# Kernel optimization log

Hardware: AMD Instinct MI355X
Metric: run time of the kernel (lower is better)

The kernel has to match this reference:

```python
import jax, jax.numpy as jnp
import numpy as np

S, B, F, D, DF, NH, FH = 1152, 2, 128, 1024, 2048, 8, 4
SEP = 1024
EPS = 1e-5

def ln(x, g, b):
    m = x.mean(-1, keepdims=True)
    v = ((x - m) ** 2).mean(-1, keepdims=True)
    return (x - m) * jax.lax.rsqrt(v + EPS) * g + b

def mha(q, k, v, wi, bi, wo, bo, nh):
    # torch MultiheadAttention, batch_first=False: inputs (L, N, E)
    E = q.shape[-1]
    hd = E // nh
    qh = (q @ wi[:E].T + bi[:E]).reshape(q.shape[0], -1, nh, hd)
    kh = (k @ wi[E:2 * E].T + bi[E:2 * E]).reshape(k.shape[0], -1, nh, hd)
    vh = (v @ wi[2 * E:].T + bi[2 * E:]).reshape(k.shape[0], -1, nh, hd)
    s = jnp.einsum('qnhd,knhd->nhqk', qh, kh) / jnp.sqrt(jnp.float32(hd))
    a = jax.nn.softmax(s, axis=-1)
    o = jnp.einsum('nhqk,knhd->qnhd', a, vh).reshape(q.shape[0], -1, E)
    return o @ wo.T + bo

def setup_inputs() -> dict:
    key = jax.random.key(0)
    it = iter(jax.random.split(key, 40))
    def p(shape, s=0.02):
        return jax.random.normal(next(it), shape, jnp.float32) * s
    z = lambda *sh: jnp.zeros(sh, jnp.float32)
    o = lambda *sh: jnp.ones(sh, jnp.float32)
    return dict(
        src=jax.random.normal(next(it), (S, B, F), jnp.float32),
        sep=SEP,
        sa_wi=p((3 * D, D)), sa_bi=z(3 * D), sa_wo=p((D, D)), sa_bo=z(D),
        fa_wi=p((3 * F, F)), fa_bi=z(3 * F), fa_wo=p((F, F)), fa_bo=z(F),
        pl1_w=p((F, 1)), pl1_b=z(F),
        pl2_w=p((DF, F)), pl2_b=z(DF),
        pl3_w=p((1, DF)), pl3_b=z(1),
        pl4_w=p((DF, F)), pl4_b=z(DF),
        pl5_w=p((D, DF)), pl5_b=z(D),
        pl6_w=p((DF, D)), pl6_b=z(DF),
        pl7_w=p((D, DF)), pl7_b=z(D),
        l1_w=p((DF, D)), l1_b=z(DF),
        l2_w=p((F, DF)), l2_b=z(F),
        pn1_g=o(F), pn1_b=z(F),
        pn2_g=o(D), pn2_b=z(D),
        n1_g=o(D), n1_b=z(D),
        n2_g=o(F), n2_b=z(F),
    )

def _forward(src, sa_wi, sa_bi, sa_wo, sa_bo, fa_wi, fa_bi, fa_wo, fa_bo,
             pl1_w, pl1_b, pl2_w, pl2_b, pl3_w, pl3_b, pl4_w, pl4_b,
             pl5_w, pl5_b, pl6_w, pl6_b, pl7_w, pl7_b, l1_w, l1_b, l2_w, l2_b,
             pn1_g, pn1_b, pn2_g, pn2_b, n1_g, n1_b, n2_g, n2_b, sep):
    Sn, Bn, Fn = src.shape
    relu = jax.nn.relu
    # feature-wise attention: 'b h w -> w (b h) 1'
    x = jnp.transpose(src, (2, 0, 1)).reshape(Fn, Sn * Bn, 1)
    x = x @ pl1_w.T + pl1_b                       # (F, S*B, emsize_f)
    x = mha(x, x, x, fa_wi, fa_bi, fa_wo, fa_bo, FH)
    x = relu(x @ pl2_w.T + pl2_b) @ pl3_w.T + pl3_b  # (F, S*B, 1)
    x = jnp.transpose(x.reshape(Fn, Sn, Bn), (1, 2, 0))  # 'w (b h) 1 -> b h w'
    src1 = ln(x + src, pn1_g, pn1_b)              # (S, B, F)
    src1_ = relu(src1 @ pl4_w.T + pl4_b) @ pl5_w.T + pl5_b  # (S, B, D)
    li = src1_[:sep]
    sl = mha(li, li, li, sa_wi, sa_bi, sa_wo, sa_bo, NH)
    sl = ln(sl + li, pn2_g, pn2_b)
    sl_ = relu(sl @ pl6_w.T + pl6_b) @ pl7_w.T + pl7_b
    sl_ = ln(sl_, pn2_g, pn2_b) + sl
    sr = mha(src1_[sep:], sl_, sl_, sa_wi, sa_bi, sa_wo, sa_bo, NH)
    src2 = jnp.concatenate([sl, sr], axis=0)      # (S, B, D)
    so = ln(src2 + src1_, n1_g, n1_b)
    ff = relu(so @ l1_w.T + l1_b) @ l2_w.T + l2_b  # (S, B, F)
    return ln(src1 + ff, n2_g, n2_b)

def reference(src, sa_wi, sa_bi, sa_wo, sa_bo, fa_wi, fa_bi, fa_wo, fa_bo,
              pl1_w, pl1_b, pl2_w, pl2_b, pl3_w, pl3_b, pl4_w, pl4_b,
              pl5_w, pl5_b, pl6_w, pl6_b, pl7_w, pl7_b, l1_w, l1_b, l2_w, l2_b,
              pn1_g, pn1_b, pn2_g, pn2_b, n1_g, n1_b, n2_g, n2_b, sep):
    return _forward(src, sa_wi, sa_bi, sa_wo, sa_bo, fa_wi, fa_bi, fa_wo, fa_bo,
                    pl1_w, pl1_b, pl2_w, pl2_b, pl3_w, pl3_b, pl4_w, pl4_b,
                    pl5_w, pl5_b, pl6_w, pl6_b, pl7_w, pl7_b, l1_w, l1_b,
                    l2_w, l2_b, pn1_g, pn1_b, pn2_g, pn2_b, n1_g, n1_b,
                    n2_g, n2_b, sep)
```

## Files before the change

### kernel.cpp

```cpp
#include <hip/hip_runtime.h>

using s16x8 = __attribute__((ext_vector_type(8))) short;
using f32x4 = __attribute__((ext_vector_type(4))) float;
typedef unsigned short ushort_t;

__device__ __forceinline__ unsigned short f2bf(float f) {
    union { float f; unsigned u; } v; v.f = f;
    unsigned u = v.u + 0x7FFFu + ((v.u >> 16) & 1u);
    return (unsigned short)(u >> 16);
}
__device__ __forceinline__ float bf2f(unsigned short h) {
    union { unsigned u; float f; } v; v.u = ((unsigned)h) << 16;
    return v.f;
}

__device__ __forceinline__ float block_reduce(float v, int op, float* lds) {
    const int lane = threadIdx.x & 63;
    const int w    = threadIdx.x >> 6;
    const int nw   = blockDim.x >> 6;
#pragma unroll
    for (int off = 32; off > 0; off >>= 1) {
        float o = __shfl_down(v, off, 64);
        v = op ? fmaxf(v, o) : (v + o);
    }
    __syncthreads();
    if (lane == 0) lds[w] = v;
    __syncthreads();
    float r = lds[0];
    for (int i = 1; i < nw; i++) r = op ? fmaxf(r, lds[i]) : (r + lds[i]);
    return r;
}

__device__ __forceinline__ void load_lds16(const void* g, void* l) {
    __builtin_amdgcn_global_load_lds(
        (const __attribute__((address_space(1))) unsigned int*)g,
        (__attribute__((address_space(3))) unsigned int*)l, 16, 0, 0);
}

struct CvtArgs { const float* src[8]; ushort_t* dst[8]; int end[8]; };

__global__ __launch_bounds__(256)
void cvt_all(CvtArgs a)
{
    int i = blockIdx.x * 256 + threadIdx.x;
    int j = 0;
    while (j < 8 && i >= a.end[j]) j++;
    if (j >= 8) return;
    int li = i - (j ? a.end[j - 1] : 0);
    float4 v = *(const float4*)&a.src[j][(size_t)li * 4];
    ushort_t u[4] = { f2bf(v.x), f2bf(v.y), f2bf(v.z), f2bf(v.w) };
    *(uint2*)&a.dst[j][(size_t)li * 4] = *(uint2*)u;
}

template<bool BKN, bool RELU>
__global__ __launch_bounds__(256, 2)
void gemm_bf16(const ushort_t* __restrict__ A, const ushort_t* __restrict__ B,
               const float* __restrict__ bias, ushort_t* __restrict__ C,
               int M, int N, int K, int lda, int ldb, int ldc,
               long sAz, long sBz, long sCz, long sA2, long sB2, long sC2,
               int zshift, float alpha)
{
    __shared__ ushort_t As[128 * 32];
    __shared__ ushort_t Bs[128 * 32];

    const int tid = threadIdx.x;
    const int z   = blockIdx.z;
    const int z1  = z & ((1 << zshift) - 1);
    const int z2  = z >> zshift;
    const int m0  = blockIdx.x * 128;
    const int n0  = blockIdx.y * 128;

    const ushort_t* Ab = A + (size_t)z1 * sAz + (size_t)z2 * sA2 + (size_t)m0 * lda;
    const ushort_t* Bb = B + (size_t)z1 * sBz + (size_t)z2 * sB2;

    const int wave = tid >> 6, lane = tid & 63;
    const int wm = (wave & 1) * 64, wn = (wave >> 1) * 64;
    const int mi = lane & 15, quad = lane >> 4;

    f32x4 acc[4][4];
#pragma unroll
    for (int i = 0; i < 4; i++)
#pragma unroll
        for (int j = 0; j < 4; j++) acc[i][j] = (f32x4)0.f;

    const int r_0 = tid >> 2,           g_0 = (tid & 3) ^ ((r_0 >> 1) & 3);
    const int r_1 = (tid + 256) >> 2,   g_1 = (tid & 3) ^ ((r_1 >> 1) & 3);
    const int bk = tid >> 3, bn = (tid & 7) * 16;

    for (int k0 = 0; k0 < K; k0 += 32) {
        load_lds16(Ab + (size_t)r_0 * lda + k0 + g_0 * 8, &As[tid * 8]);
        load_lds16(Ab + (size_t)r_1 * lda + k0 + g_1 * 8, &As[(tid + 256) * 8]);
        if (!BKN) {
            const ushort_t* Bb2 = Bb + (size_t)n0 * ldb;
            load_lds16(Bb2 + (size_t)r_0 * ldb + k0 + g_0 * 8, &Bs[tid * 8]);
            load_lds16(Bb2 + (size_t)r_1 * ldb + k0 + g_1 * 8, &Bs[(tid + 256) * 8]);
        } else {
#pragma unroll
            for (int c = 0; c < 2; c++) {
                s16x8 v = *(const s16x8*)(Bb + (size_t)(k0 + bk) * ldb + n0 + bn + c * 8);
#pragma unroll
                for (int j = 0; j < 8; j++) {
                    int nr = bn + c * 8 + j;
                    Bs[nr * 32 + (((bk >> 3) ^ ((nr >> 1) & 3)) * 8) + (bk & 7)] = (ushort_t)v[j];
                }
            }
        }
        __syncthreads();

        s16x8 af[4], bfr[4];
#pragma unroll
        for (int t = 0; t < 4; t++) {
            int r = wm + t * 16 + mi;
            af[t] = *(const s16x8*)&As[r * 32 + ((quad ^ ((r >> 1) & 3)) * 8)];
        }
#pragma unroll
        for (int t = 0; t < 4; t++) {
            int r = wn + t * 16 + mi;
            bfr[t] = *(const s16x8*)&Bs[r * 32 + ((quad ^ ((r >> 1) & 3)) * 8)];
        }
#pragma unroll
        for (int tm = 0; tm < 4; tm++)
#pragma unroll
            for (int tn = 0; tn < 4; tn++)
                acc[tm][tn] = __builtin_amdgcn_mfma_f32_16x16x32_bf16(af[tm], bfr[tn], acc[tm][tn], 0, 0, 0);
        __syncthreads();
    }

#pragma unroll
    for (int tn = 0; tn < 4; tn++) {
        int col = n0 + wn + tn * 16 + mi;
        float bv = bias ? bias[col] : 0.f;
#pragma unroll
        for (int tm = 0; tm < 4; tm++) {
#pragma unroll
            for (int r = 0; r < 4; r++) {
                int row = m0 + wm + tm * 16 + quad * 4 + r;
                float v = acc[tm][tn][r] * alpha + bv;
                if (RELU) v = fmaxf(v, 0.f);
                C[(size_t)z1 * sCz + (size_t)z2 * sC2 + (size_t)row * ldc + col] = f2bf(v);
            }
        }
    }
}

__global__ void precomp1(const float* __restrict__ fa_wi, const float* __restrict__ fa_bi,
                         const float* __restrict__ pl1_w, const float* __restrict__ pl1_b,
                         float* __restrict__ consts)
{
    int j = threadIdx.x;
    if (j < 384) {
        float u = 0.f, v = 0.f;
        for (int k = 0; k < 128; k++) {
            float w = fa_wi[j * 128 + k];
            u = fmaf(w, pl1_w[k], u);
            v = fmaf(w, pl1_b[k], v);
        }
        consts[j]       = u;
        consts[512 + j] = v + fa_bi[j];
    }
}

__global__ void precomp2(const float* __restrict__ fa_wo, const float* __restrict__ fa_bo,
                         float* __restrict__ consts)
{
    int tid = threadIdx.x;
    const float* u = consts;
    const float* v = consts + 512;
    if (tid < 16) {
        int h = tid >> 2, w = tid & 3;
        const float* ql = (w < 2) ? u : v;
        const float* kr = ((w & 1) == 0) ? u : v;
        float acc = 0.f;
        for (int d = 0; d < 32; d++) acc += ql[h * 32 + d] * kr[128 + h * 32 + d];
        consts[1024 + tid] = acc * 0.17677669529663687f;
    }
#pragma unroll
    for (int h = 0; h < 4; h++) {
        float acc = 0.f;
        for (int d = 0; d < 32; d++)
            acc = fmaf(fa_wo[tid * 128 + h * 32 + d], u[256 + h * 32 + d], acc);
        consts[1088 + h * 128 + tid] = acc;
    }
    float c0 = fa_bo[tid];
    for (int idx = 0; idx < 128; idx++)
        c0 = fmaf(fa_wo[tid * 128 + idx], v[256 + idx], c0);
    consts[1600 + tid] = c0;
}

__global__ void precomp3(const float* __restrict__ pl2_w, const float* __restrict__ pl2_b,
                         const float* __restrict__ consts, ushort_t* __restrict__ Gb)
{
    int m = blockIdx.x * 256 + threadIdx.x;
    const float* wv = consts + 1088;
    const float* c0 = consts + 1600;
    float a0 = 0.f, ah[4] = {0.f, 0.f, 0.f, 0.f};
    for (int j = 0; j < 128; j++) {
        float w = pl2_w[m * 128 + j];
        ah[0] = fmaf(w, wv[0 * 128 + j], ah[0]);
        ah[1] = fmaf(w, wv[1 * 128 + j], ah[1]);
        ah[2] = fmaf(w, wv[2 * 128 + j], ah[2]);
        ah[3] = fmaf(w, wv[3 * 128 + j], ah[3]);
        a0    = fmaf(w, c0[j], a0);
    }
    ushort_t* row = Gb + m * 32;
#pragma unroll
    for (int h = 0; h < 4; h++) row[h] = f2bf(ah[h]);
    row[4] = f2bf(a0 + pl2_b[m]);
#pragma unroll
    for (int j = 5; j < 32; j++) row[j] = 0;
}

__global__ __launch_bounds__(256, 3)
void feat_mlp_ln(const float* __restrict__ src, const float* __restrict__ consts,
                 const ushort_t* __restrict__ Gb, const float* __restrict__ pl3_w,
                 const float* __restrict__ pl3_b, const float* __restrict__ pn1_g,
                 const float* __restrict__ pn1_b, ushort_t* __restrict__ src1)
{
    __shared__ ushort_t As[128 * 32];
    __shared__ ushort_t Bs[256 * 32];
    __shared__ float sv[128];
    __shared__ float ypart[2][128];
    __shared__ float red[4];

    const int n   = blockIdx.x;
    const int tid = threadIdx.x;
    const int f   = tid & 127;
    const int hp  = tid >> 7;

    *(uint4*)&As[tid * 16]     = (uint4){0, 0, 0, 0};
    *(uint4*)&As[tid * 16 + 8] = (uint4){0, 0, 0, 0};
    if (tid < 128) sv[f] = src[n * 128 + f];
    __syncthreads();

    const float si = sv[f];
    const bool act = (tid < 128);
    float S1 = block_reduce(act ? si : 0.f, 0, red);
    float S2 = block_reduce(act ? si * si : 0.f, 0, red);
    float S3 = block_reduce(act ? si * si * si : 0.f, 0, red);
    float S4 = block_reduce(act ? si * si * si * si : 0.f, 0, red);
    float amax = block_reduce(act ? fabsf(si) : 0.f, 1, red);

    float ph[2];
#pragma unroll
    for (int hh = 0; hh < 2; hh++) {
        const int h = hp * 2 + hh;
        ph[hh] = consts[1024 + h * 4 + 0] * si + consts[1024 + h * 4 + 2];
    }
    float pmax = block_reduce(fmaxf(fabsf(ph[0]), fabsf(ph[1])), 1, red);

    float tt[2];
    if (pmax * amax < 0.25f) {
#pragma unroll
        for (int hh = 0; hh < 2; hh++) {
            float p = ph[hh];
            float num = fmaf(p, fmaf(p, fmaf(p, S4 * (1.f / 6.f), 0.5f * S3), S2), S1);
            float den = fmaf(p, fmaf(p, fmaf(p, S3 * (1.f / 6.f), 0.5f * S2), S1), 128.f);
            tt[hh] = num / den;
        }
    } else {
        float smax = block_reduce(act ? si : -3.4e38f, 1, red);
        float smin = -block_reduce(act ? -si : -3.4e38f, 1, red);
#pragma unroll
        for (int hh = 0; hh < 2; hh++) {
            float p = ph[hh];
            float m = fmaxf(p * smax, p * smin);
            float l = 0.f, t = 0.f;
            for (int j = 0; j < 128; j++) {
                float e = __expf(fmaf(p, sv[j], -m));
                l += e; t = fmaf(e, sv[j], t);
            }
            tt[hh] = t / l;
        }
    }

    {
        int base = f * 32 + (((f >> 1) & 3) * 8);
        As[base + hp * 2 + 0] = f2bf(tt[0]);
        As[base + hp * 2 + 1] = f2bf(tt[1]);
        if (act) As[base + 4] = 0x3F80;
    }
    __syncthreads();

    const int wave = tid >> 6, lane = tid & 63;
    const int wm = (wave & 1) * 64, wn = (wave >> 1) * 64;
    const int mi = lane & 15, quad = lane >> 4;

    s16x8 af[4];
#pragma unroll
    for (int t = 0; t < 4; t++) {
        int r = wm + t * 16 + mi;
        af[t] = *(const s16x8*)&As[r * 32 + ((quad ^ ((r >> 1) & 3)) * 8)];
    }

    float partial[4][4];
#pragma unroll
    for (int i = 0; i < 4; i++)
#pragma unroll
        for (int j = 0; j < 4; j++) partial[i][j] = 0.f;

    for (int cchunk = 0; cchunk < 8; cchunk++) {
        const ushort_t* Gc = Gb + cchunk * 256 * 32;
#pragma unroll
        for (int p = 0; p < 4; p++) {
            int ci = tid + p * 256;
            int r  = ci >> 2;
            int g  = (ci & 3) ^ ((r >> 1) & 3);
            load_lds16(Gc + (size_t)r * 32 + g * 8, &Bs[ci * 8]);
        }
        __syncthreads();

#pragma unroll
        for (int sub = 0; sub < 2; sub++) {
            s16x8 bfr[4];
#pragma unroll
            for (int t = 0; t < 4; t++) {
                int r = sub * 128 + wn + t * 16 + mi;
                bfr[t] = *(const s16x8*)&Bs[r * 32 + ((quad ^ ((r >> 1) & 3)) * 8)];
            }

            f32x4 acc[4][4];
#pragma unroll
            for (int tm = 0; tm < 4; tm++)
#pragma unroll
                for (int tn = 0; tn < 4; tn++)
                    acc[tm][tn] = __builtin_amdgcn_mfma_f32_16x16x32_bf16(af[tm], bfr[tn], (f32x4)0.f, 0, 0, 0);

#pragma unroll
            for (int tn = 0; tn < 4; tn++) {
                float w = pl3_w[cchunk * 256 + sub * 128 + wn + tn * 16 + mi];
#pragma unroll
                for (int tm = 0; tm < 4; tm++)
#pragma unroll
                    for (int r = 0; r < 4; r++)
                        partial[tm][r] = fmaf(fmaxf(acc[tm][tn][r], 0.f), w, partial[tm][r]);
            }
        }
        __syncthreads();
    }

#pragma unroll
    for (int tm = 0; tm < 4; tm++)
#pragma unroll
        for (int r = 0; r < 4; r++) {
            float v = partial[tm][r];
            v += __shfl_xor(v, 8);
            v += __shfl_xor(v, 4);
            v += __shfl_xor(v, 2);
            v += __shfl_xor(v, 1);
            if (mi == 0) ypart[wave >> 1][wm + tm * 16 + quad * 4 + r] = v;
        }
    __syncthreads();

    float yv = 0.f;
    if (act)
        yv = ypart[0][f] + ypart[1][f] + pl3_b[0] + sv[f];
    float s  = block_reduce(yv, 0, red);
    float ss = block_reduce(yv * yv, 0, red);
    float mean = s * (1.f / 128.f);
    float var  = ss * (1.f / 128.f) - mean * mean;
    float inv  = rsqrtf(var + 1e-5f);
    if (act)
        src1[n * 128 + f] = f2bf((yv - mean) * inv * pn1_g[f] + pn1_b[f]);
}

template<bool OUTF32>
__global__ void ln_bf16(const ushort_t* __restrict__ a, const ushort_t* __restrict__ b,
                        const ushort_t* __restrict__ post, const float* __restrict__ g,
                        const float* __restrict__ beta, void* __restrict__ out, int D)
{
    __shared__ float red[4];
    const size_t row = blockIdx.x;
    const int tid = threadIdx.x;
    const int nit = D / blockDim.x;
    const ushort_t* ap = a + row * D;
    const ushort_t* bp = b ? b + row * D : nullptr;
    float xr[4];
    float s = 0.f, ss = 0.f;
    for (int i = 0; i < nit; i++) {
        int idx = i * blockDim.x + tid;
        float x = bf2f(ap[idx]) + (bp ? bf2f(bp[idx]) : 0.f);
        xr[i] = x; s += x; ss = fmaf(x, x, ss);
    }
    s  = block_reduce(s, 0, red);
    ss = block_reduce(ss, 0, red);
    float mean = s / D, var = ss / D - mean * mean;
    float inv = rsqrtf(var + 1e-5f);
    const ushort_t* pp = post ? post + row * D : nullptr;
    for (int i = 0; i < nit; i++) {
        int idx = i * blockDim.x + tid;
        float v = (xr[i] - mean) * inv * g[idx] + beta[idx];
        if (pp) v += bf2f(pp[idx]);
        if (OUTF32) ((float*)out)[row * D + idx] = v;
        else        ((ushort_t*)out)[row * D + idx] = f2bf(v);
    }
}

__global__ void ln_cat(const ushort_t* __restrict__ a1, const ushort_t* __restrict__ a2,
                       int split, const ushort_t* __restrict__ b,
                       const float* __restrict__ g, const float* __restrict__ beta,
                       ushort_t* __restrict__ out, int D)
{
    __shared__ float red[4];
    const int row = blockIdx.x;
    const int tid = threadIdx.x;
    const int nit = D / blockDim.x;
    const ushort_t* ap = (row < split) ? a1 + (size_t)row * D : a2 + (size_t)(row - split) * D;
    const ushort_t* bp = b + (size_t)row * D;
    float xr[4];
    float s = 0.f, ss = 0.f;
    for (int i = 0; i < nit; i++) {
        int idx = i * blockDim.x + tid;
        float x = bf2f(ap[idx]) + bf2f(bp[idx]);
        xr[i] = x; s += x; ss = fmaf(x, x, ss);
    }
    s  = block_reduce(s, 0, red);
    ss = block_reduce(ss, 0, red);
    float mean = s / D, var = ss / D - mean * mean;
    float inv = rsqrtf(var + 1e-5f);
    for (int i = 0; i < nit; i++) {
        int idx = i * blockDim.x + tid;
        out[(size_t)row * D + idx] = f2bf((xr[i] - mean) * inv * g[idx] + beta[idx]);
    }
}

__global__ __launch_bounds__(256)
void softmax_bf16(ushort_t* __restrict__ S)
{
    __shared__ float red[4];
    const size_t row = blockIdx.x;
    ushort_t* p = S + row * 1024;
    const int tid = threadIdx.x;
    uint2 u = *(const uint2*)&p[tid * 4];
    ushort_t* us = (ushort_t*)&u;
    float xr[4];
    float mx = -3.4e38f;
#pragma unroll
    for (int i = 0; i < 4; i++) { xr[i] = bf2f(us[i]); mx = fmaxf(mx, xr[i]); }
    mx = block_reduce(mx, 1, red);
    float sum = 0.f;
#pragma unroll
    for (int i = 0; i < 4; i++) { xr[i] = __expf(xr[i] - mx); sum += xr[i]; }
    sum = block_reduce(sum, 0, red);
    float inv = 1.f / sum;
#pragma unroll
    for (int i = 0; i < 4; i++) us[i] = f2bf(xr[i] * inv);
    *(uint2*)&p[tid * 4] = u;
}

static inline void gemm_go(hipStream_t s, const ushort_t* A, const ushort_t* B,
                           const float* bias, ushort_t* C,
                           int M, int N, int K, int lda, int ldb, int ldc,
                           long sAz, long sBz, long sCz, int Z, float alpha,
                           bool bkn, bool relu,
                           long sA2 = 0, long sB2 = 0, long sC2 = 0, int zshift = 0)
{
    dim3 g(M / 128, N / 128, Z), b(256);
    if (bkn)       gemm_bf16<true,  false><<<g, b, 0, s>>>(A, B, bias, C, M, N, K, lda, ldb, ldc, sAz, sBz, sCz, sA2, sB2, sC2, zshift, alpha);
    else if (relu) gemm_bf16<false, true ><<<g, b, 0, s>>>(A, B, bias, C, M, N, K, lda, ldb, ldc, sAz, sBz, sCz, sA2, sB2, sC2, zshift, alpha);
    else           gemm_bf16<false, false><<<g, b, 0, s>>>(A, B, bias, C, M, N, K, lda, ldb, ldc, sAz, sBz, sCz, sA2, sB2, sC2, zshift, alpha);
}

extern "C" void kernel_launch(void* const* d_in, const int* in_sizes, int n_in,
                              void* d_out, int out_size, void* d_ws, size_t ws_size,
                              hipStream_t stream)
{
    const float* src   = (const float*)d_in[0];
    const float* sa_wi = (const float*)d_in[2];
    const float* sa_bi = (const float*)d_in[3];
    const float* sa_wo = (const float*)d_in[4];
    const float* sa_bo = (const float*)d_in[5];
    const float* fa_wi = (const float*)d_in[6];
    const float* fa_bi = (const float*)d_in[7];
    const float* fa_wo = (const float*)d_in[8];
    const float* fa_bo = (const float*)d_in[9];
    const float* pl1_w = (const float*)d_in[10];
    const float* pl1_b = (const float*)d_in[11];
    const float* pl2_w = (const float*)d_in[12];
    const float* pl2_b = (const float*)d_in[13];
    const float* pl3_w = (const float*)d_in[14];
    const float* pl3_b = (const float*)d_in[15];
    const float* pl4_w = (const float*)d_in[16];
    const float* pl4_b = (const float*)d_in[17];
    const float* pl5_w = (const float*)d_in[18];
    const float* pl5_b = (const float*)d_in[19];
    const float* pl6_w = (const float*)d_in[20];
    const float* pl6_b = (const float*)d_in[21];
    const float* pl7_w = (const float*)d_in[22];
    const float* pl7_b = (const float*)d_in[23];
    const float* l1_w  = (const float*)d_in[24];
    const float* l1_b  = (const float*)d_in[25];
    const float* l2_w  = (const float*)d_in[26];
    const float* l2_b  = (const float*)d_in[27];
    const float* pn1_g = (const float*)d_in[28];
    const float* pn1_b = (const float*)d_in[29];
    const float* pn2_g = (const float*)d_in[30];
    const float* pn2_b = (const float*)d_in[31];
    const float* n1_g  = (const float*)d_in[32];
    const float* n1_b  = (const float*)d_in[33];
    const float* n2_g  = (const float*)d_in[34];
    const float* n2_b  = (const float*)d_in[35];

    float* ws  = (float*)d_ws;
    float* out = (float*)d_out;

    float* CONSTS = ws;
    ushort_t* wsb = (ushort_t*)(ws + 16384);
    ushort_t* SAWIb  = wsb + 0;
    ushort_t* SAWOb  = wsb + 3145728;
    ushort_t* PL4b   = wsb + 4194304;
    ushort_t* PL5b   = wsb + 4456448;
    ushort_t* PL6b   = wsb + 6553600;
    ushort_t* PL7b   = wsb + 8650752;
    ushort_t* L1b    = wsb + 10747904;
    ushort_t* L2b    = wsb + 12845056;
    ushort_t* Gbb    = wsb + 13107200;
    ushort_t* SRC1b  = wsb + 13172736;
    ushort_t* HBIGb  = wsb + 13467648;
    ushort_t* SRC1_b = wsb + 18186240;
    ushort_t* QKVb   = wsb + 20545536;
    ushort_t* SBUFb  = wsb + 27623424;
    ushort_t* OBUFb  = wsb + 44400640;
    ushort_t* SLb    = wsb + 46497792;
    ushort_t* SLPb   = wsb + 48594944;
    ushort_t* SOb    = wsb + 50692096;
    ushort_t* FFb    = wsb + 53051392;

    {
        CvtArgs a;
        const float* srcs[8] = { sa_wi, sa_wo, pl4_w, pl5_w, pl6_w, pl7_w, l1_w, l2_w };
        ushort_t*    dsts[8] = { SAWIb, SAWOb, PL4b, PL5b, PL6b, PL7b, L1b, L2b };
        int          ns[8]   = { 3145728, 1048576, 262144, 2097152, 2097152, 2097152, 2097152, 262144 };
        int cum = 0;
        for (int i = 0; i < 8; i++) { a.src[i] = srcs[i]; a.dst[i] = dsts[i]; cum += ns[i] / 4; a.end[i] = cum; }
        cvt_all<<<(cum + 255) / 256, 256, 0, stream>>>(a);
    }

    precomp1<<<1, 384, 0, stream>>>(fa_wi, fa_bi, pl1_w, pl1_b, CONSTS);
    precomp2<<<1, 128, 0, stream>>>(fa_wo, fa_bo, CONSTS);
    precomp3<<<8, 256, 0, stream>>>(pl2_w, pl2_b, CONSTS, Gbb);
    feat_mlp_ln<<<2304, 256, 0, stream>>>(src, CONSTS, Gbb, pl3_w, pl3_b, pn1_g, pn1_b, SRC1b);

    gemm_go(stream, SRC1b, PL4b, pl4_b, HBIGb, 2304, 2048, 128, 128, 128, 2048, 0, 0, 0, 1, 1.f, false, true);
    gemm_go(stream, HBIGb, PL5b, pl5_b, SRC1_b, 2304, 1024, 2048, 2048, 2048, 1024, 0, 0, 0, 1, 1.f, false, false);

    gemm_go(stream, SRC1_b, SAWIb, sa_bi, QKVb, 2304, 3072, 1024, 1024, 1024, 3072, 0, 0, 0, 1, 1.f, false, false);
    const float iscale = 0.08838834764831845f;
    gemm_go(stream, QKVb, QKVb + 1024, nullptr, SBUFb,
            1024, 1024, 128, 6144, 6144, 1024, 128, 128, 1048576, 16, iscale, false, false,
            3072, 3072, 8388608, 3);
    softmax_bf16<<<16384, 256, 0, stream>>>(SBUFb);
    gemm_go(stream, SBUFb, QKVb + 2048, nullptr, OBUFb,
            1024, 128, 1024, 1024, 6144, 2048, 1048576, 128, 128, 16, 1.f, true, false,
            8388608, 3072, 1024, 3);
    gemm_go(stream, OBUFb, SAWOb, sa_bo, HBIGb, 2048, 1024, 1024, 1024, 1024, 1024, 0, 0, 0, 1, 1.f, false, false);
    ln_bf16<false><<<2048, 256, 0, stream>>>(HBIGb, SRC1_b, nullptr, pn2_g, pn2_b, SLb, 1024);

    gemm_go(stream, SLb, PL6b, pl6_b, HBIGb, 2048, 2048, 1024, 1024, 1024, 2048, 0, 0, 0, 1, 1.f, false, true);
    gemm_go(stream, HBIGb, PL7b, pl7_b, OBUFb, 2048, 1024, 2048, 2048, 2048, 1024, 0, 0, 0, 1, 1.f, false, false);
    ln_bf16<false><<<2048, 256, 0, stream>>>(OBUFb, nullptr, SLb, pn2_g, pn2_b, SLPb, 1024);

    ushort_t* KV2 = SBUFb;
    ushort_t* S2  = SBUFb + 4456448;
    ushort_t* SR  = SBUFb + 6553600;
    gemm_go(stream, SLPb, SAWIb + 1024 * 1024, sa_bi + 1024, KV2, 2048, 2048, 1024, 1024, 1024, 2048, 0, 0, 0, 1, 1.f, false, false);
    gemm_go(stream, QKVb + 2048 * 3072, KV2, nullptr, S2,
            128, 1024, 128, 6144, 4096, 1024, 128, 128, 131072, 16, iscale, false, false,
            3072, 2048, 1048576, 3);
    softmax_bf16<<<2048, 256, 0, stream>>>(S2);
    gemm_go(stream, S2, KV2 + 1024, nullptr, OBUFb,
            128, 128, 1024, 1024, 4096, 2048, 131072, 128, 128, 16, 1.f, true, false,
            1048576, 2048, 1024, 3);
    gemm_go(stream, OBUFb, SAWOb, sa_bo, SR, 256, 1024, 1024, 1024, 1024, 1024, 0, 0, 0, 1, 1.f, false, false);

    ln_cat<<<2304, 256, 0, stream>>>(SLb, SR, 2048, SRC1_b, n1_g, n1_b, SOb, 1024);

    gemm_go(stream, SOb, L1b, l1_b, HBIGb, 2304, 2048, 1024, 1024, 1024, 2048, 0, 0, 0, 1, 1.f, false, true);
    gemm_go(stream, HBIGb, L2b, l2_b, FFb, 2304, 128, 2048, 2048, 2048, 128, 0, 0, 0, 1, 1.f, false, false);
    ln_bf16<true><<<2304, 128, 0, stream>>>(FFb, SRC1b, nullptr, n2_g, n2_b, out, 128);
}
```

Measured before the change: 665.4 us.

## Pre-transpose V for attention GEMMs and shrink feature MLP K padding

Adds a transpose kernel that writes V in N-major layout, so the attention P·V GEMMs can use the async LDS-load path instead of the scalar scattered B-transposed load. The BKN template variant is removed. Separately, the feature-MLP kernel now packs its tiny K=5 operand into 8-wide rows, preloads the whole G matrix and pl3 weights into LDS once, and runs a single-tile MFMA loop instead of 32-wide padded chunks with repeated syncs. Costs two extra transpose launches and more LDS per block in feat_mlp_ln, which may lower occupancy.

Result: faster. 639.3 us (-3.9%).

```diff
diff --git a/kernel.cpp b/kernel.cpp
--- a/kernel.cpp
+++ b/kernel.cpp
@@ -52,7 +52,7 @@
     *(uint2*)&a.dst[j][(size_t)li * 4] = *(uint2*)u;
 }
 
-template<bool BKN, bool RELU>
+template<bool RELU>
 __global__ __launch_bounds__(256, 2)
 void gemm_bf16(const ushort_t* __restrict__ A, const ushort_t* __restrict__ B,
                const float* __restrict__ bias, ushort_t* __restrict__ C,
@@ -71,7 +71,7 @@
     const int n0  = blockIdx.y * 128;
 
     const ushort_t* Ab = A + (size_t)z1 * sAz + (size_t)z2 * sA2 + (size_t)m0 * lda;
-    const ushort_t* Bb = B + (size_t)z1 * sBz + (size_t)z2 * sB2;
+    const ushort_t* Bb = B + (size_t)z1 * sBz + (size_t)z2 * sB2 + (size_t)n0 * ldb;
 
     const int wave = tid >> 6, lane = tid & 63;
     const int wm = (wave & 1) * 64, wn = (wave >> 1) * 64;
@@ -85,26 +85,12 @@
 
     const int r_0 = tid >> 2,           g_0 = (tid & 3) ^ ((r_0 >> 1) & 3);
     const int r_1 = (tid + 256) >> 2,   g_1 = (tid & 3) ^ ((r_1 >> 1) & 3);
-    const int bk = tid >> 3, bn = (tid & 7) * 16;
 
     for (int k0 = 0; k0 < K; k0 += 32) {
         load_lds16(Ab + (size_t)r_0 * lda + k0 + g_0 * 8, &As[tid * 8]);
         load_lds16(Ab + (size_t)r_1 * lda + k0 + g_1 * 8, &As[(tid + 256) * 8]);
-        if (!BKN) {
-            const ushort_t* Bb2 = Bb + (size_t)n0 * ldb;
-            load_lds16(Bb2 + (size_t)r_0 * ldb + k0 + g_0 * 8, &Bs[tid * 8]);
-            load_lds16(Bb2 + (size_t)r_1 * ldb + k0 + g_1 * 8, &Bs[(tid + 256) * 8]);
-        } else {
-#pragma unroll
-            for (int c = 0; c < 2; c++) {
-                s16x8 v = *(const s16x8*)(Bb + (size_t)(k0 + bk) * ldb + n0 + bn + c * 8);
-#pragma unroll
-                for (int j = 0; j < 8; j++) {
-                    int nr = bn + c * 8 + j;
-                    Bs[nr * 32 + (((bk >> 3) ^ ((nr >> 1) & 3)) * 8) + (bk & 7)] = (ushort_t)v[j];
-                }
-            }
-        }
+        load_lds16(Bb + (size_t)r_0 * ldb + k0 + g_0 * 8, &Bs[tid * 8]);
+        load_lds16(Bb + (size_t)r_1 * ldb + k0 + g_1 * 8, &Bs[(tid + 256) * 8]);
         __syncthreads();
 
         s16x8 af[4], bfr[4];
@@ -140,6 +126,32 @@
                 C[(size_t)z1 * sCz + (size_t)z2 * sC2 + (size_t)row * ldc + col] = f2bf(v);
             }
         }
+    }
+}
+
+__global__ __launch_bounds__(256)
+void transp128(const ushort_t* __restrict__ in, ushort_t* __restrict__ out,
+               int ldin, long inz1, long inz2, long outz)
+{
+    __shared__ ushort_t T[64][136];
+    const int z = blockIdx.z, z1 = z & 7, z2 = z >> 3;
+    const int n0 = blockIdx.x * 64;
+    const ushort_t* ip = in + (size_t)z1 * inz1 + (size_t)z2 * inz2;
+    const int rr = threadIdx.x >> 2, cg = (threadIdx.x & 3) * 32;
+#pragma unroll
+    for (int c = 0; c < 4; c++) {
+        s16x8 v = *(const s16x8*)(ip + (size_t)(n0 + rr) * ldin + cg + c * 8);
+        *(s16x8*)&T[rr][cg + c * 8] = v;
+    }
+    __syncthreads();
+    const int d = threadIdx.x >> 1, j0 = (threadIdx.x & 1) * 32;
+    ushort_t* op = out + (size_t)z * outz + (size_t)d * 1024 + n0 + j0;
+#pragma unroll
+    for (int c = 0; c < 4; c++) {
+        s16x8 v;
+#pragma unroll
+        for (int j = 0; j < 8; j++) v[j] = (short)T[j0 + c * 8 + j][d];
+        *(s16x8*)(op + c * 8) = v;
     }
 }
 
@@ -202,12 +214,12 @@
         ah[3] = fmaf(w, wv[3 * 128 + j], ah[3]);
         a0    = fmaf(w, c0[j], a0);
     }
-    ushort_t* row = Gb + m * 32;
+    ushort_t row[8];
 #pragma unroll
     for (int h = 0; h < 4; h++) row[h] = f2bf(ah[h]);
     row[4] = f2bf(a0 + pl2_b[m]);
-#pragma unroll
-    for (int j = 5; j < 32; j++) row[j] = 0;
+    row[5] = row[6] = row[7] = 0;
+    *(uint4*)&Gb[m * 8] = *(uint4*)row;
 }
 
 __global__ __launch_bounds__(256, 3)
@@ -216,24 +228,31 @@
                  const float* __restrict__ pl3_b, const float* __restrict__ pn1_g,
                  const float* __restrict__ pn1_b, ushort_t* __restrict__ src1)
 {
-    __shared__ ushort_t As[128 * 32];
-    __shared__ ushort_t Bs[256 * 32];
-    __shared__ float sv[128];
-    __shared__ float ypart[2][128];
-    __shared__ float red[4];
+    __shared__ ushort_t Gs[2048 * 8];
+    __shared__ ushort_t Ts[128 * 8];
+    __shared__ float    wlds[2048];
+    __shared__ float    sv[128];
+    __shared__ float    ypart[2][128];
+    __shared__ float    red[4];
 
     const int n   = blockIdx.x;
     const int tid = threadIdx.x;
     const int f   = tid & 127;
     const int hp  = tid >> 7;
-
-    *(uint4*)&As[tid * 16]     = (uint4){0, 0, 0, 0};
-    *(uint4*)&As[tid * 16 + 8] = (uint4){0, 0, 0, 0};
-    if (tid < 128) sv[f] = src[n * 128 + f];
+    const bool act = (tid < 128);
+
+#pragma unroll
+    for (int p = 0; p < 8; p++) {
+        int ci = tid + p * 256;
+        load_lds16(Gb + (size_t)ci * 8, &Gs[ci * 8]);
+    }
+    load_lds16(pl3_w + tid * 4,          &wlds[tid * 4]);
+    load_lds16(pl3_w + (tid + 256) * 4,  &wlds[(tid + 256) * 4]);
+
+    if (act) sv[f] = src[n * 128 + f];
     __syncthreads();
 
     const float si = sv[f];
-    const bool act = (tid < 128);
     float S1 = block_reduce(act ? si : 0.f, 0, red);
     float S2 = block_reduce(act ? si * si : 0.f, 0, red);
     float S3 = block_reduce(act ? si * si * si : 0.f, 0, red);
@@ -273,23 +292,23 @@
         }
     }
 
-    {
-        int base = f * 32 + (((f >> 1) & 3) * 8);
-        As[base + hp * 2 + 0] = f2bf(tt[0]);
-        As[base + hp * 2 + 1] = f2bf(tt[1]);
-        if (act) As[base + 4] = 0x3F80;
+    Ts[f * 8 + hp * 2 + 0] = f2bf(tt[0]);
+    Ts[f * 8 + hp * 2 + 1] = f2bf(tt[1]);
+    if (act) {
+        Ts[f * 8 + 4] = 0x3F80;
+        Ts[f * 8 + 5] = 0; Ts[f * 8 + 6] = 0; Ts[f * 8 + 7] = 0;
     }
     __syncthreads();
 
     const int wave = tid >> 6, lane = tid & 63;
-    const int wm = (wave & 1) * 64, wn = (wave >> 1) * 64;
+    const int mhalf = wave >> 1, wm = (wave & 1) * 64;
     const int mi = lane & 15, quad = lane >> 4;
 
     s16x8 af[4];
 #pragma unroll
     for (int t = 0; t < 4; t++) {
-        int r = wm + t * 16 + mi;
-        af[t] = *(const s16x8*)&As[r * 32 + ((quad ^ ((r >> 1) & 3)) * 8)];
+        s16x8 v = *(const s16x8*)&Ts[(wm + t * 16 + mi) * 8];
+        af[t] = (quad == 0) ? v : (s16x8)0;
     }
 
     float partial[4][4];
@@ -298,44 +317,20 @@
 #pragma unroll
         for (int j = 0; j < 4; j++) partial[i][j] = 0.f;
 
-    for (int cchunk = 0; cchunk < 8; cchunk++) {
-        const ushort_t* Gc = Gb + cchunk * 256 * 32;
-#pragma unroll
-        for (int p = 0; p < 4; p++) {
-            int ci = tid + p * 256;
-            int r  = ci >> 2;
-            int g  = (ci & 3) ^ ((r >> 1) & 3);
-            load_lds16(Gc + (size_t)r * 32 + g * 8, &Bs[ci * 8]);
-        }
-        __syncthreads();
-
-#pragma unroll
-        for (int sub = 0; sub < 2; sub++) {
-            s16x8 bfr[4];
-#pragma unroll
-            for (int t = 0; t < 4; t++) {
-                int r = sub * 128 + wn + t * 16 + mi;
-                bfr[t] = *(const s16x8*)&Bs[r * 32 + ((quad ^ ((r >> 1) & 3)) * 8)];
-            }
-
-            f32x4 acc[4][4];
-#pragma unroll
-            for (int tm = 0; tm < 4; tm++)
-#pragma unroll
-                for (int tn = 0; tn < 4; tn++)
-                    acc[tm][tn] = __builtin_amdgcn_mfma_f32_16x16x32_bf16(af[tm], bfr[tn], (f32x4)0.f, 0, 0, 0);
-
-#pragma unroll
-            for (int tn = 0; tn < 4; tn++) {
-                float w = pl3_w[cchunk * 256 + sub * 128 + wn + tn * 16 + mi];
-#pragma unroll
-                for (int tm = 0; tm < 4; tm++)
-#pragma unroll
-                    for (int r = 0; r < 4; r++)
-                        partial[tm][r] = fmaf(fmaxf(acc[tm][tn][r], 0.f), w, partial[tm][r]);
-            }
-        }
-        __syncthreads();
+#pragma unroll 2
+    for (int mt = 0; mt < 64; mt++) {
+        const int m0 = mhalf * 1024 + mt * 16;
+        s16x8 bfr = *(const s16x8*)&Gs[(m0 + mi) * 8];
+        f32x4 acc[4];
+#pragma unroll
+        for (int tm = 0; tm < 4; tm++)
+            acc[tm] = __builtin_amdgcn_mfma_f32_16x16x32_bf16(af[tm], bfr, (f32x4)0.f, 0, 0, 0);
+        float w = wlds[m0 + mi];
+#pragma unroll
+        for (int tm = 0; tm < 4; tm++)
+#pragma unroll
+            for (int r = 0; r < 4; r++)
+                partial[tm][r] = fmaf(fmaxf(acc[tm][r], 0.f), w, partial[tm][r]);
     }
 
 #pragma unroll
@@ -347,7 +342,7 @@
             v += __shfl_xor(v, 4);
             v += __shfl_xor(v, 2);
             v += __shfl_xor(v, 1);
-            if (mi == 0) ypart[wave >> 1][wm + tm * 16 + quad * 4 + r] = v;
+            if (mi == 0) ypart[mhalf][wm + tm * 16 + quad * 4 + r] = v;
         }
     __syncthreads();
 
@@ -451,13 +446,12 @@
                            const float* bias, ushort_t* C,
                            int M, int N, int K, int lda, int ldb, int ldc,
                            long sAz, long sBz, long sCz, int Z, float alpha,
-                           bool bkn, bool relu,
+                           bool relu,
                            long sA2 = 0, long sB2 = 0, long sC2 = 0, int zshift = 0)
 {
     dim3 g(M / 128, N / 128, Z), b(256);
-    if (bkn)       gemm_bf16<true,  false><<<g, b, 0, s>>>(A, B, bias, C, M, N, K, lda, ldb, ldc, sAz, sBz, sCz, sA2, sB2, sC2, zshift, alpha);
-    else if (relu) gemm_bf16<false, true ><<<g, b, 0, s>>>(A, B, bias, C, M, N, K, lda, ldb, ldc, sAz, sBz, sCz, sA2, sB2, sC2, zshift, alpha);
-    else           gemm_bf16<false, false><<<g, b, 0, s>>>(A, B, bias, C, M, N, K, lda, ldb, ldc, sAz, sBz, sCz, sA2, sB2, sC2, zshift, alpha);
+    if (relu) gemm_bf16<true ><<<g, b, 0, s>>>(A, B, bias, C, M, N, K, lda, ldb, ldc, sAz, sBz, sCz, sA2, sB2, sC2, zshift, alpha);
+    else      gemm_bf16<false><<<g, b, 0, s>>>(A, B, bias, C, M, N, K, lda, ldb, ldc, sAz, sBz, sCz, sA2, sB2, sC2, zshift, alpha);
 }
 
 extern "C" void kernel_launch(void* const* d_in, const int* in_sizes, int n_in,
@@ -540,41 +534,45 @@
     precomp3<<<8, 256, 0, stream>>>(pl2_w, pl2_b, CONSTS, Gbb);
     feat_mlp_ln<<<2304, 256, 0, stream>>>(src, CONSTS, Gbb, pl3_w, pl3_b, pn1_g, pn1_b, SRC1b);
 
-    gemm_go(stream, SRC1b, PL4b, pl4_b, HBIGb, 2304, 2048, 128, 128, 128, 2048, 0, 0, 0, 1, 1.f, false, true);
-    gemm_go(stream, HBIGb, PL5b, pl5_b, SRC1_b, 2304, 1024, 2048, 2048, 2048, 1024, 0, 0, 0, 1, 1.f, false, false);
-
-    gemm_go(stream, SRC1_b, SAWIb, sa_bi, QKVb, 2304, 3072, 1024, 1024, 1024, 3072, 0, 0, 0, 1, 1.f, false, false);
+    gemm_go(stream, SRC1b, PL4b, pl4_b, HBIGb, 2304, 2048, 128, 128, 128, 2048, 0, 0, 0, 1, 1.f, true);
+    gemm_go(stream, HBIGb, PL5b, pl5_b, SRC1_b, 2304, 1024, 2048, 2048, 2048, 1024, 0, 0, 0, 1, 1.f, false);
+
+    gemm_go(stream, SRC1_b, SAWIb, sa_bi, QKVb, 2304, 3072, 1024, 1024, 1024, 3072, 0, 0, 0, 1, 1.f, false);
     const float iscale = 0.08838834764831845f;
+    ushort_t* VT1 = HBIGb;
+    transp128<<<dim3(16, 1, 16), 256, 0, stream>>>(QKVb + 2048, VT1, 6144, 128, 3072, 131072);
     gemm_go(stream, QKVb, QKVb + 1024, nullptr, SBUFb,
-            1024, 1024, 128, 6144, 6144, 1024, 128, 128, 1048576, 16, iscale, false, false,
+            1024, 1024, 128, 6144, 6144, 1024, 128, 128, 1048576, 16, iscale, false,
             3072, 3072, 8388608, 3);
     softmax_bf16<<<16384, 256, 0, stream>>>(SBUFb);
-    gemm_go(stream, SBUFb, QKVb + 2048, nullptr, OBUFb,
-            1024, 128, 1024, 1024, 6144, 2048, 1048576, 128, 128, 16, 1.f, true, false,
-            8388608, 3072, 1024, 3);
-    gemm_go(stream, OBUFb, SAWOb, sa_bo, HBIGb, 2048, 1024, 1024, 1024, 1024, 1024, 0, 0, 0, 1, 1.f, false, false);
+    gemm_go(stream, SBUFb, VT1, nullptr, OBUFb,
+            1024, 128, 1024, 1024, 1024, 2048, 1048576, 131072, 128, 16, 1.f, false,
+            8388608, 1048576, 1024, 3);
+    gemm_go(stream, OBUFb, SAWOb, sa_bo, HBIGb, 2048, 1024, 1024, 1024, 1024, 1024, 0, 0, 0, 1, 1.f, false);
     ln_bf16<false><<<2048, 256, 0, stream>>>(HBIGb, SRC1_b, nullptr, pn2_g, pn2_b, SLb, 1024);
 
-    gemm_go(stream, SLb, PL6b, pl6_b, HBIGb, 2048, 2048, 1024, 1024, 1024, 2048, 0, 0, 0, 1, 1.f, false, true);
-    gemm_go(stream, HBIGb, PL7b, pl7_b, OBUFb, 2048, 1024, 2048, 2048, 2048, 1024, 0, 0, 0, 1, 1.f, false, false);
+    gemm_go(stream, SLb, PL6b, pl6_b, HBIGb, 2048, 2048, 1024, 1024, 1024, 2048, 0, 0, 0, 1, 1.f, true);
+    gemm_go(stream, HBIGb, PL7b, pl7_b, OBUFb, 2048, 1024, 2048, 2048, 2048, 1024, 0, 0, 0, 1, 1.f, false);
     ln_bf16<false><<<2048, 256, 0, stream>>>(OBUFb, nullptr, SLb, pn2_g, pn2_b, SLPb, 1024);
 
     ushort_t* KV2 = SBUFb;
     ushort_t* S2  = SBUFb + 4456448;
     ushort_t* SR  = SBUFb + 6553600;
-    gemm_go(stream, SLPb, SAWIb + 1024 * 1024, sa_bi + 1024, KV2, 2048, 2048, 1024, 1024, 1024, 2048, 0, 0, 0, 1, 1.f, false, false);
+    gemm_go(stream, SLPb, SAWIb + 1024 * 1024, sa_bi + 1024, KV2, 2048, 2048, 1024, 1024, 1024, 2048, 0, 0, 0, 1, 1.f, false);
+    ushort_t* VT2 = HBIGb;
+    transp128<<<dim3(16, 1, 16), 256, 0, stream>>>(KV2 + 1024, VT2, 4096, 128, 2048, 131072);
     gemm_go(stream, QKVb + 2048 * 3072, KV2, nullptr, S2,
-            128, 1024, 128, 6144, 4096, 1024, 128, 128, 131072, 16, iscale, false, false,
+            128, 1024, 128, 6144, 4096, 1024, 128, 128, 131072, 16, iscale, false,
             3072, 2048, 1048576, 3);
     softmax_bf16<<<2048, 256, 0, stream>>>(S2);
-    gemm_go(stream, S2, KV2 + 1024, nullptr, OBUFb,
-            128, 128, 1024, 1024, 4096, 2048, 131072, 128, 128, 16, 1.f, true, false,
-            1048576, 2048, 1024, 3);
-    gemm_go(stream, OBUFb, SAWOb, sa_bo, SR, 256, 1024, 1024, 1024, 1024, 1024, 0, 0, 0, 1, 1.f, false, false);
+    gemm_go(stream, S2, VT2, nullptr, OBUFb,
+            128, 128, 1024, 1024, 1024, 2048, 131072, 131072, 128, 16, 1.f, false,
+            1048576, 1048576, 1024, 3);
+    gemm_go(stream, OBUFb, SAWOb, sa_bo, SR, 256, 1024, 1024, 1024, 1024, 1024, 0, 0, 0, 1, 1.f, false);
 
     ln_cat<<<2304, 256, 0, stream>>>(SLb, SR, 2048, SRC1_b, n1_g, n1_b, SOb, 1024);
 
-    gemm_go(stream, SOb, L1b, l1_b, HBIGb, 2304, 2048, 1024, 1024, 1024, 2048, 0, 0, 0, 1, 1.f, false, true);
-    gemm_go(stream, HBIGb, L2b, l2_b, FFb, 2304, 128, 2048, 2048, 2048, 128, 0, 0, 0, 1, 1.f, false, false);
+    gemm_go(stream, SOb, L1b, l1_b, HBIGb, 2304, 2048, 1024, 1024, 1024, 2048, 0, 0, 0, 1, 1.f, true);
+    gemm_go(stream, HBIGb, L2b, l2_b, FFb, 2304, 128, 2048, 2048, 2048, 128, 0, 0, 0, 1, 1.f, false);
     ln_bf16<true><<<2304, 128, 0, stream>>>(FFb, SRC1b, nullptr, n2_g, n2_b, out, 128);
 }
```
